# Kernel optimization log

Measured on AMD Instinct MI355X. Metric: run time of the kernel, lower is better.

## Reference

```python
import jax, jax.numpy as jnp
import numpy as np

B, T, V, H, L = 2048, 128, 256, 20, 15  # batch, seq_len, vocab, hidden, max_label


def setup_inputs() -> dict:
    key = jax.random.key(0)
    ks = jax.random.split(key, 8)
    g = lambda k, shape, s: (jax.random.normal(k, shape, jnp.float32) * s)
    return {
        "x": jax.random.randint(ks[0], (B, T), 0, V, dtype=jnp.int32),
        "W0": g(ks[1], (V, 3 * H), 0.06),   # input kernel layer 0 [V, 3H] (z|r|h)
        "U0": g(ks[2], (H, 3 * H), 0.2),    # recurrent kernel layer 0
        "b0i": jnp.zeros((3 * H,), jnp.float32),  # input bias (reset_after=True split bias)
        "b0r": jnp.zeros((3 * H,), jnp.float32),  # recurrent bias
        "W1": g(ks[3], (H, 3 * H), 0.2),
        "U1": g(ks[4], (H, 3 * H), 0.2),
        "b1i": jnp.zeros((3 * H,), jnp.float32),
        "b1r": jnp.zeros((3 * H,), jnp.float32),
        "Wd": g(ks[5], (H, L), 0.2),
        "bd": jnp.zeros((L,), jnp.float32),
        "drop_rate": 0,  # identity dropout (deterministic reference)
    }


def _gru_cell(h, xw, U, br):
    # Keras GRUCell with reset_after=True:
    #   xw = x @ W + b_in  (precomputed), rec = h @ U + b_rec
    rec = h @ U + br
    xz, xr, xh = jnp.split(xw, 3, axis=-1)
    rz, rr, rh = jnp.split(rec, 3, axis=-1)
    z = jax.nn.sigmoid(xz + rz)
    r = jax.nn.sigmoid(xr + rr)
    hh = jnp.tanh(xh + r * rh)
    return z * h + (1.0 - z) * hh


def reference(x, W0, U0, b0i, b0r, W1, U1, b1i, b1r, Wd, bd, drop_rate):
    # one_hot(x) @ W0 == gather rows of W0 (same math, no [B,T,V] materialization)
    xW0 = W0[x] + b0i                 # [B, T, 3H]
    xW0 = jnp.swapaxes(xW0, 0, 1)     # [T, B, 3H] for scan over time

    def step(carry, xw_t):
        h0, h1 = carry
        h0 = _gru_cell(h0, xw_t, U0, b0r)
        xw1 = h0 @ W1 + b1i
        h1 = _gru_cell(h1, xw1, U1, b1r)
        return (h0, h1), None

    h0 = jnp.zeros((x.shape[0], H), W0.dtype)
    h1 = jnp.zeros((x.shape[0], H), W0.dtype)
    (h0, h1), _ = jax.lax.scan(step, (h0, h1), xW0)
    # tf.nn.dropout with rate 0 is the identity
    out = h1
    logits = jax.nn.softmax(out @ Wd + bd, axis=-1)  # [B, L]
    return logits
```

## Files before the change

### kernel.cpp

```cpp
#include <hip/hip_runtime.h>


#define BB 2048
#define TT 128
#define HH 20
#define LL 15
#define H3 60

typedef float v2f __attribute__((ext_vector_type(2)));

#if __has_builtin(__builtin_amdgcn_exp2f)
#define EXP2(x) __builtin_amdgcn_exp2f(x)
#else
#define EXP2(x) exp2f(x)
#endif

__device__ __forceinline__ float bclane(float v, int k) {
    return __int_as_float(__builtin_amdgcn_readlane(__float_as_int(v), k));
}
__device__ __forceinline__ float dpp_rshr1(float v) {
    return __int_as_float(__builtin_amdgcn_update_dpp(
        0, __float_as_int(v), 0x111, 0xF, 0xF, true));
}
__device__ __forceinline__ float dpp_rshr2(float v) {
    return __int_as_float(__builtin_amdgcn_update_dpp(
        0, __float_as_int(v), 0x112, 0xF, 0xF, true));
}
__device__ __forceinline__ float fast_rcp(float x) { return __builtin_amdgcn_rcpf(x); }
#define PIN(v) asm volatile("" : "+v"(v))

extern "C" __global__ __launch_bounds__(512, 4)
void gru2_kernel(const int* __restrict__ x, const float* __restrict__ W0,
                 const float* __restrict__ U0, const float* __restrict__ b0i,
                 const float* __restrict__ b0r, const float* __restrict__ W1,
                 const float* __restrict__ U1, const float* __restrict__ b1i,
                 const float* __restrict__ b1r, const float* __restrict__ Wd,
                 const float* __restrict__ bd, float* __restrict__ out)
{
    const int lane = threadIdx.x & 63;
    const int w    = threadIdx.x >> 6;
    const int g    = w & 3;
    const int role = w >> 2;
    const int batch = blockIdx.x * 4 + g;

    const int row = lane >> 4;
    const int pos = lane & 15;
    const int pc  = (pos < 15) ? pos : 14;
    const int u   = pc / 3;
    const int p3  = pc % 3;
    const int j   = row * 5 + u;
    const bool home = (pos < 15) && (p3 == 2);
    const int col = p3 * 20 + j;

    const float gsc = (p3 == 2) ? -2.8853900817779268f : -1.4426950408889634f;

    __shared__ __align__(16) float h0s[4][2][24];
    __shared__ __align__(16) float h1s[4][24];
    float* h0a = &h0s[g][0][0];
    float* h0b = &h0s[g][1][0];
    float* h1a = &h1s[g][0];
    const float4* q0a = (const float4*)h0a;
    const float4* q0b = (const float4*)h0b;
    const float4* q1a = (const float4*)h1a;

    v2f wA[10], wB[10];
    v2f biasP;
    v2f biasT;
    float xbias = 0.f;
    float4 cP[5], cT[5];
    float h0 = 0.f, h1 = 0.f;

    int tokn2 = 0, tAlo = 0, tAhi = 0;
    float xw_cur = 0.f, xw_nxt = 0.f;

    if (role == 0) {
#pragma unroll
        for (int q = 0; q < 10; ++q) {
            const int k0 = (2 * q) * H3, k1 = (2 * q + 1) * H3;
            wA[q] = v2f{U0[k0 + col] * gsc, U0[k1 + col] * gsc};
        }
        biasP = v2f{b0r[col] * gsc, 0.f};
        xbias = b0i[col] * gsc;
        const int* xrow = x + batch * TT;
        tAlo = xrow[lane];
        tAhi = xrow[64 + lane];
        tokn2  = __builtin_amdgcn_readlane(tAlo, 2);
        xw_cur = fmaf(W0[__builtin_amdgcn_readlane(tAlo, 0) * H3 + col], gsc, xbias);
        xw_nxt = W0[__builtin_amdgcn_readlane(tAlo, 1) * H3 + col];
    } else {
#pragma unroll
        for (int q = 0; q < 10; ++q) {
            const int k0 = (2 * q) * H3, k1 = (2 * q + 1) * H3;
            wA[q] = v2f{W1[k0 + col] * gsc, W1[k1 + col] * gsc};
            wB[q] = v2f{U1[k0 + col] * gsc, U1[k1 + col] * gsc};
        }
        biasP = v2f{b1r[col] * gsc, 0.f};
        biasT = v2f{b1i[col] * gsc, 0.f};
    }
#pragma unroll
    for (int q = 0; q < 10; ++q) { PIN(wA[q]); PIN(wB[q]); }
#pragma unroll
    for (int q = 0; q < 5; ++q) cP[q] = float4{0.f, 0.f, 0.f, 0.f};

#define DOT1(C, P, BIASV, OUT)                                                \
    {                                                                         \
        v2f aa = __builtin_elementwise_fma(v2f{C[0].x, C[0].y}, P[0], BIASV); \
        v2f ab = v2f{C[0].z, C[0].w} * P[1];                                  \
        _Pragma("unroll")                                                     \
        for (int q = 1; q < 5; ++q) {                                         \
            aa = __builtin_elementwise_fma(v2f{C[q].x, C[q].y}, P[2 * q], aa);\
            ab = __builtin_elementwise_fma(v2f{C[q].z, C[q].w}, P[2 * q + 1], ab);\
        }                                                                     \
        const v2f t_ = aa + ab;                                               \
        OUT = t_.x + t_.y;                                                    \
    }
#define GATES(XW, REC, H)                                                     \
    {                                                                         \
        const float e_  = EXP2((XW) + (REC));                                 \
        const float t_  = fast_rcp(1.f + e_);                                 \
        const float rv_ = dpp_rshr1(t_);                                      \
        const float zv_ = dpp_rshr2(t_);                                      \
        const float eh_ = EXP2(fmaf(rv_, (REC), (XW)));                       \
        const float th_ = fast_rcp(1.f + eh_);                                \
        const float hh_ = fmaf(2.f, th_, -1.f);                               \
        H = fmaf(zv_, (H) - hh_, hh_);                                        \
    }

    for (int t = 0; t <= TT; ++t) {
        __syncthreads();
        if (role == 0) {
            if (t < TT) {
                const int t3 = (t + 3 < TT) ? (t + 3) : (TT - 1);
                const float pf = W0[tokn2 * H3 + col];
                const int tokn3 =
                    __builtin_amdgcn_readlane(t3 < 64 ? tAlo : tAhi, t3 & 63);
                float rec0;
                DOT1(cP, wA, biasP, rec0);
                GATES(xw_cur, rec0, h0);
                float* hw = (t & 1) ? h0b : h0a;
                if (home) hw[j] = h0;
                const float4* qs = (t & 1) ? q0b : q0a;
#pragma unroll
                for (int q = 0; q < 5; ++q) cP[q] = qs[q];
                xw_cur = fmaf(xw_nxt, gsc, xbias);
                xw_nxt = pf; tokn2 = tokn3;
            }
        } else {
            if (t > 0) {
                const float4* qs = ((t - 1) & 1) ? q0b : q0a;
#pragma unroll
                for (int q = 0; q < 5; ++q) cT[q] = qs[q];
                float rec1;
                DOT1(cP, wB, biasP, rec1);
                float xw1;
                DOT1(cT, wA, biasT, xw1);
                GATES(xw1, rec1, h1);
                if (home) h1a[j] = h1;
#pragma unroll
                for (int q = 0; q < 5; ++q) cP[q] = q1a[q];
            }
        }
    }

    if (role == 1) {
        const int l = lane < LL ? lane : LL - 1;
        float acc = bd[l];
#pragma unroll
        for (int k = 0; k < HH; ++k)
            acc = fmaf(h1a[k], Wd[k * LL + l], acc);

        float m = acc;
#pragma unroll
        for (int i = 0; i < LL; ++i) m = fmaxf(m, bclane(acc, i));
        const float e = __expf(acc - m);
        float s = 0.f;
#pragma unroll
        for (int i = 0; i < LL; ++i) s += bclane(e, i);
        const float pr = e * fast_rcp(s);

        if (lane < LL) out[batch * LL + lane] = pr;
    }
}

extern "C" void kernel_launch(void* const* d_in, const int* in_sizes, int n_in,
                              void* d_out, int out_size, void* d_ws, size_t ws_size,
                              hipStream_t stream) {
    const int*   x   = (const int*)  d_in[0];
    const float* W0  = (const float*)d_in[1];
    const float* U0  = (const float*)d_in[2];
    const float* b0i = (const float*)d_in[3];
    const float* b0r = (const float*)d_in[4];
    const float* W1  = (const float*)d_in[5];
    const float* U1  = (const float*)d_in[6];
    const float* b1i = (const float*)d_in[7];
    const float* b1r = (const float*)d_in[8];
    const float* Wd  = (const float*)d_in[9];
    const float* bd  = (const float*)d_in[10];
    float* out = (float*)d_out;

    dim3 grid(BB / 4), block(512);
    hipLaunchKernelGGL(gru2_kernel, grid, block, 0, stream,
                       x, W0, U0, b0i, b0r, W1, U1, b1i, b1r, Wd, bd, out);
}
```

Measured before the change: 137.8 us.

## Replace per-step block barriers with LDS ring buffer and spin-wait producer-consumer flags

The layer-0 and layer-1 waves stop synchronising with __syncthreads every timestep. Layer 0 now writes each h0 into a per-batch LDS ring holding all timesteps and publishes progress through a volatile counter, and layer 1 spin-waits on that counter. This lets layer 0 run ahead without waiting for layer 1, taking the barrier cost off the critical path. It relies on intra-wave LDS ordering and on only a compiler fence before the flag store, so cross-wave visibility is a correctness risk. The ring also raises LDS use to about 49KB per block, which may limit occupancy, and spinning waves consume issue slots.

```diff
diff --git a/kernel.cpp b/kernel.cpp
--- a/kernel.cpp
+++ b/kernel.cpp
@@ -28,6 +28,30 @@
 }
 __device__ __forceinline__ float fast_rcp(float x) { return __builtin_amdgcn_rcpf(x); }
 #define PIN(v) asm volatile("" : "+v"(v))
+#define LDSFENCE() asm volatile("" ::: "memory")
+
+#define GATES(XW, REC, H)                                                     \
+    {                                                                         \
+        const float e_  = EXP2((XW) + (REC));                                 \
+        const float t_  = fast_rcp(1.f + e_);                                 \
+        const float rv_ = dpp_rshr1(t_);                                      \
+        const float zv_ = dpp_rshr2(t_);                                      \
+        const float eh_ = EXP2(fmaf(rv_, (REC), (XW)));                       \
+        const float th_ = fast_rcp(1.f + eh_);                                \
+        const float hh_ = fmaf(2.f, th_, -1.f);                               \
+        H = fmaf(zv_, (H) - hh_, hh_);                                        \
+    }
+#define DOTD(C, P, BIASV, OUT)                                                \
+    {                                                                         \
+        v2f aa = BIASV, ab = v2f{0.f, 0.f};                                   \
+        _Pragma("unroll")                                                     \
+        for (int q = 0; q < 5; ++q) {                                         \
+            aa = __builtin_elementwise_fma(v2f{C[q].x, C[q].y}, P[2 * q], aa);\
+            ab = __builtin_elementwise_fma(v2f{C[q].z, C[q].w}, P[2 * q + 1], ab);\
+        }                                                                     \
+        const v2f t_ = aa + ab;                                               \
+        OUT = t_.x + t_.y;                                                    \
+    }
 
 extern "C" __global__ __launch_bounds__(512, 4)
 void gru2_kernel(const int* __restrict__ x, const float* __restrict__ W0,
@@ -54,132 +78,126 @@
 
     const float gsc = (p3 == 2) ? -2.8853900817779268f : -1.4426950408889634f;
 
-    __shared__ __align__(16) float h0s[4][2][24];
+    __shared__ __align__(16) float ring[4][TT][24];
     __shared__ __align__(16) float h1s[4][24];
-    float* h0a = &h0s[g][0][0];
-    float* h0b = &h0s[g][1][0];
-    float* h1a = &h1s[g][0];
-    const float4* q0a = (const float4*)h0a;
-    const float4* q0b = (const float4*)h0b;
-    const float4* q1a = (const float4*)h1a;
-
-    v2f wA[10], wB[10];
-    v2f biasP;
-    v2f biasT;
-    float xbias = 0.f;
-    float4 cP[5], cT[5];
-    float h0 = 0.f, h1 = 0.f;
-
-    int tokn2 = 0, tAlo = 0, tAhi = 0;
-    float xw_cur = 0.f, xw_nxt = 0.f;
+    __shared__ int cnts[4];
+    float* myring = &ring[g][0][0];
+    float* h1buf  = &h1s[g][0];
+    volatile int* vcnt = &cnts[g];
+
+    if (threadIdx.x < 4) cnts[threadIdx.x] = 0;
+    __syncthreads();
 
     if (role == 0) {
+        v2f u0p[10];
 #pragma unroll
         for (int q = 0; q < 10; ++q) {
             const int k0 = (2 * q) * H3, k1 = (2 * q + 1) * H3;
-            wA[q] = v2f{U0[k0 + col] * gsc, U0[k1 + col] * gsc};
-        }
-        biasP = v2f{b0r[col] * gsc, 0.f};
-        xbias = b0i[col] * gsc;
+            u0p[q] = v2f{U0[k0 + col] * gsc, U0[k1 + col] * gsc};
+        }
+#pragma unroll
+        for (int q = 0; q < 10; ++q) PIN(u0p[q]);
+        const float bi0 = b0i[col] * gsc, br0 = b0r[col] * gsc;
+        const v2f br0v = v2f{br0, 0.f};
+
         const int* xrow = x + batch * TT;
-        tAlo = xrow[lane];
-        tAhi = xrow[64 + lane];
-        tokn2  = __builtin_amdgcn_readlane(tAlo, 2);
-        xw_cur = fmaf(W0[__builtin_amdgcn_readlane(tAlo, 0) * H3 + col], gsc, xbias);
-        xw_nxt = W0[__builtin_amdgcn_readlane(tAlo, 1) * H3 + col];
-    } else {
-#pragma unroll
-        for (int q = 0; q < 10; ++q) {
-            const int k0 = (2 * q) * H3, k1 = (2 * q + 1) * H3;
-            wA[q] = v2f{W1[k0 + col] * gsc, W1[k1 + col] * gsc};
-            wB[q] = v2f{U1[k0 + col] * gsc, U1[k1 + col] * gsc};
-        }
-        biasP = v2f{b1r[col] * gsc, 0.f};
-        biasT = v2f{b1i[col] * gsc, 0.f};
-    }
-#pragma unroll
-    for (int q = 0; q < 10; ++q) { PIN(wA[q]); PIN(wB[q]); }
-#pragma unroll
-    for (int q = 0; q < 5; ++q) cP[q] = float4{0.f, 0.f, 0.f, 0.f};
-
-#define DOT1(C, P, BIASV, OUT)                                                \
-    {                                                                         \
-        v2f aa = __builtin_elementwise_fma(v2f{C[0].x, C[0].y}, P[0], BIASV); \
-        v2f ab = v2f{C[0].z, C[0].w} * P[1];                                  \
-        _Pragma("unroll")                                                     \
-        for (int q = 1; q < 5; ++q) {                                         \
-            aa = __builtin_elementwise_fma(v2f{C[q].x, C[q].y}, P[2 * q], aa);\
-            ab = __builtin_elementwise_fma(v2f{C[q].z, C[q].w}, P[2 * q + 1], ab);\
-        }                                                                     \
-        const v2f t_ = aa + ab;                                               \
-        OUT = t_.x + t_.y;                                                    \
-    }
-#define GATES(XW, REC, H)                                                     \
-    {                                                                         \
-        const float e_  = EXP2((XW) + (REC));                                 \
-        const float t_  = fast_rcp(1.f + e_);                                 \
-        const float rv_ = dpp_rshr1(t_);                                      \
-        const float zv_ = dpp_rshr2(t_);                                      \
-        const float eh_ = EXP2(fmaf(rv_, (REC), (XW)));                       \
-        const float th_ = fast_rcp(1.f + eh_);                                \
-        const float hh_ = fmaf(2.f, th_, -1.f);                               \
-        H = fmaf(zv_, (H) - hh_, hh_);                                        \
-    }
-
-    for (int t = 0; t <= TT; ++t) {
-        __syncthreads();
-        if (role == 0) {
-            if (t < TT) {
-                const int t3 = (t + 3 < TT) ? (t + 3) : (TT - 1);
-                const float pf = W0[tokn2 * H3 + col];
-                const int tokn3 =
-                    __builtin_amdgcn_readlane(t3 < 64 ? tAlo : tAhi, t3 & 63);
-                float rec0;
-                DOT1(cP, wA, biasP, rec0);
-                GATES(xw_cur, rec0, h0);
-                float* hw = (t & 1) ? h0b : h0a;
-                if (home) hw[j] = h0;
-                const float4* qs = (t & 1) ? q0b : q0a;
-#pragma unroll
-                for (int q = 0; q < 5; ++q) cP[q] = qs[q];
-                xw_cur = fmaf(xw_nxt, gsc, xbias);
-                xw_nxt = pf; tokn2 = tokn3;
-            }
-        } else {
-            if (t > 0) {
-                const float4* qs = ((t - 1) & 1) ? q0b : q0a;
-#pragma unroll
-                for (int q = 0; q < 5; ++q) cT[q] = qs[q];
-                float rec1;
-                DOT1(cP, wB, biasP, rec1);
-                float xw1;
-                DOT1(cT, wA, biasT, xw1);
-                GATES(xw1, rec1, h1);
-                if (home) h1a[j] = h1;
-#pragma unroll
-                for (int q = 0; q < 5; ++q) cP[q] = q1a[q];
-            }
-        }
-    }
-
-    if (role == 1) {
-        const int l = lane < LL ? lane : LL - 1;
-        float acc = bd[l];
-#pragma unroll
-        for (int k = 0; k < HH; ++k)
-            acc = fmaf(h1a[k], Wd[k * LL + l], acc);
-
-        float m = acc;
-#pragma unroll
-        for (int i = 0; i < LL; ++i) m = fmaxf(m, bclane(acc, i));
-        const float e = __expf(acc - m);
-        float s = 0.f;
-#pragma unroll
-        for (int i = 0; i < LL; ++i) s += bclane(e, i);
-        const float pr = e * fast_rcp(s);
-
-        if (lane < LL) out[batch * LL + lane] = pr;
-    }
+        const int tokA = xrow[lane];
+        const int tokB = xrow[64 + lane];
+        int tokn2 = __builtin_amdgcn_readlane(tokA, 2);
+        float xw_cur = fmaf(W0[__builtin_amdgcn_readlane(tokA, 0) * H3 + col], gsc, bi0);
+        float xw_nxt = W0[__builtin_amdgcn_readlane(tokA, 1) * H3 + col];
+
+        float h0 = 0.f;
+        float rec0 = br0;
+        float4 c0[5];
+
+#pragma unroll 2
+        for (int t = 0; t < TT; ++t) {
+            const int t3 = (t + 3 < TT) ? (t + 3) : (TT - 1);
+            const float pf = W0[tokn2 * H3 + col];
+            const int tokn3 =
+                __builtin_amdgcn_readlane(t3 < 64 ? tokA : tokB, t3 & 63);
+
+            GATES(xw_cur, rec0, h0);
+            float* slot = myring + t * 24;
+            if (home) slot[j] = h0;
+            LDSFENCE();
+            if (lane == 63) *vcnt = t + 1;
+            const float4* sq = (const float4*)slot;
+#pragma unroll
+            for (int q = 0; q < 5; ++q) c0[q] = sq[q];
+
+            xw_cur = fmaf(xw_nxt, gsc, bi0);
+            xw_nxt = pf; tokn2 = tokn3;
+
+            DOTD(c0, u0p, br0v, rec0);
+        }
+        return;
+    }
+
+    v2f w1p[10], u1p[10];
+#pragma unroll
+    for (int q = 0; q < 10; ++q) {
+        const int k0 = (2 * q) * H3, k1 = (2 * q + 1) * H3;
+        w1p[q] = v2f{W1[k0 + col] * gsc, W1[k1 + col] * gsc};
+        u1p[q] = v2f{U1[k0 + col] * gsc, U1[k1 + col] * gsc};
+    }
+#pragma unroll
+    for (int q = 0; q < 10; ++q) { PIN(w1p[q]); PIN(u1p[q]); }
+    const float bi1 = b1i[col] * gsc, br1 = b1r[col] * gsc;
+    const v2f bi1v = v2f{bi1, 0.f}, br1v = v2f{br1, 0.f};
+
+    float h1 = 0.f;
+    float4 c0[5], c1[5];
+    float xw1, rec1;
+
+    while (*vcnt < 1) {}
+    {
+        const float4* sq = (const float4*)myring;
+#pragma unroll
+        for (int q = 0; q < 5; ++q) c0[q] = sq[q];
+        DOTD(c0, w1p, bi1v, xw1);
+        rec1 = br1;
+    }
+
+#pragma unroll 2
+    for (int t = 0; t < TT; ++t) {
+        if (t < TT - 1) {
+            while (*vcnt < t + 2) {}
+            const float4* sq = (const float4*)(myring + (t + 1) * 24);
+#pragma unroll
+            for (int q = 0; q < 5; ++q) c0[q] = sq[q];
+        }
+
+        GATES(xw1, rec1, h1);
+        if (home) h1buf[j] = h1;
+        LDSFENCE();
+        const float4* q1 = (const float4*)h1buf;
+#pragma unroll
+        for (int q = 0; q < 5; ++q) c1[q] = q1[q];
+
+        if (t < TT - 1) {
+            DOTD(c0, w1p, bi1v, xw1);
+            DOTD(c1, u1p, br1v, rec1);
+        }
+    }
+
+    const int l = lane < LL ? lane : LL - 1;
+    float acc = bd[l];
+#pragma unroll
+    for (int k = 0; k < HH; ++k)
+        acc = fmaf(h1buf[k], Wd[k * LL + l], acc);
+
+    float m = acc;
+#pragma unroll
+    for (int i = 0; i < LL; ++i) m = fmaxf(m, bclane(acc, i));
+    const float e = __expf(acc - m);
+    float s = 0.f;
+#pragma unroll
+    for (int i = 0; i < LL; ++i) s += bclane(e, i);
+    const float pr = e * fast_rcp(s);
+
+    if (lane < LL) out[batch * LL + lane] = pr;
 }
 
 extern "C" void kernel_launch(void* const* d_in, const int* in_sizes, int n_in,
```

New measurement: 130.6 us. -5.2%, faster.
